# Performance work log

Measured on AMD Instinct MI355X. Metric: run time of the kernel, lower is better.

Reference implementation:

```python
import jax, jax.numpy as jnp
import numpy as np

N_TOK = 384
VOCAB = 50000
N_POS = 52
WDIM = 512
HDIM = 1024
FEAT_DIM = 3 * 16  # np.repeat([len,start,end],16)


def setup_inputs() -> dict:
    key = jax.random.key(0)
    ks = jax.random.split(key, 10)
    s = 0.02  # init scale
    return {
        "sentence": jax.random.randint(ks[0], (N_TOK,), 0, VOCAB),
        "pos_tags": jax.random.randint(ks[1], (N_TOK,), 0, N_POS),
        "We_wrd": jax.random.normal(ks[2], (VOCAB, WDIM), jnp.float32) * s,
        "We_pos": jax.random.normal(ks[3], (N_POS, WDIM), jnp.float32) * s,
        "W_dan1": jax.random.normal(ks[4], (2 * WDIM, HDIM), jnp.float32) * s,
        "b_dan1": jnp.zeros((HDIM,), jnp.float32),
        "W_dan2": jax.random.normal(ks[5], (HDIM, HDIM), jnp.float32) * s,
        "b_dan2": jnp.zeros((HDIM,), jnp.float32),
        "W_s1": jax.random.normal(ks[6], (HDIM + FEAT_DIM, HDIM), jnp.float32) * s,
        "b_s1": jnp.zeros((HDIM,), jnp.float32),
        "W_s2": jax.random.normal(ks[7], (HDIM, 1), jnp.float32) * s,
        "b_s2": jnp.zeros((1,), jnp.float32),
    }


def reference(sentence, pos_tags, We_wrd, We_pos, W_dan1, b_dan1, W_dan2, b_dan2, W_s1, b_s1, W_s2, b_s2):
    n = sentence.shape[0]
    # per-token embedding: concat(pos, word) as in score() with use_pos=True -> [n, 2*wdim]
    emb = jnp.concatenate([We_pos[pos_tags], We_wrd[sentence]], axis=-1)
    # prefix sums so every span mean is O(1): pref[k] = sum of emb[:k]
    pref = jnp.concatenate([jnp.zeros((1, emb.shape[1]), emb.dtype), jnp.cumsum(emb, axis=0)], axis=0)
    # all spans (i, j) with i <= j, as in the double loop over i..n-1, j..n-1
    i_idx, j_idx = np.triu_indices(n)  # static shapes, S = n(n+1)/2
    i_idx = jnp.asarray(i_idx)
    j_idx = jnp.asarray(j_idx)
    end = j_idx + 1
    length = (end - i_idx).astype(emb.dtype)
    # DAN encoder: mean of span embeddings -> 2 relu layers (config['layer']=2)
    mean = (pref[end] - pref[i_idx]) / length[:, None]            # [S, 2*wdim]
    h = jax.nn.relu(mean @ W_dan1 + b_dan1)                        # [S, hdim]
    h = jax.nn.relu(h @ W_dan2 + b_dan2)                           # [S, hdim]
    # phrase feats: np.repeat([len, start, end], 16) -> [S, 48]
    feats = jnp.repeat(jnp.stack([length, i_idx.astype(emb.dtype), end.astype(emb.dtype)], axis=1), 16, axis=1)
    rep = jnp.concatenate([h, feats], axis=1)                      # [S, hdim+48]
    # Wpscore MLP: Linear(ph_dim+48 -> hdim) + relu, Linear(hdim -> 1)
    h2 = jax.nn.relu(rep @ W_s1 + b_s1)
    scores = (h2 @ W_s2 + b_s2)[:, 0]                              # [S]
    return scores
```

## Files before the change

kernel.cpp:

```cpp
#include <hip/hip_runtime.h>

#define NTOK  384
#define SPANS 73920
#define MTILES 584
#define MPAD  (MTILES * 128)
#define HD    1024
#define BK    32
#define KTS   (HD / BK)
#define YSLICE ((size_t)NTOK * HD)

typedef unsigned short u16;
typedef __attribute__((ext_vector_type(8))) short short8;
typedef __attribute__((ext_vector_type(4))) float floatx4;

#define VMCNT_IMM(N) (((N) & 0xF) | (((N) >> 4) << 14) | (0x7 << 4) | (0xF << 8))

__device__ __forceinline__ u16 f2bu(float x) {
  union { float f; unsigned u; } un; un.f = x;
  unsigned r = un.u + 0x7fffu + ((un.u >> 16) & 1u);
  return (u16)(r >> 16);
}

__device__ __forceinline__ void gld_lds16(const void* g, void* l) {
  __builtin_amdgcn_global_load_lds(
      (const __attribute__((address_space(1))) void*)g,
      (__attribute__((address_space(3))) void*)l, 16, 0, 0);
}

__global__ void prep_misc(const int* __restrict__ sent, const int* __restrict__ pos,
                          const float* __restrict__ Wwrd, const float* __restrict__ Wpos,
                          u16* __restrict__ embB,
                          int* __restrict__ spI, int* __restrict__ spE, float* __restrict__ spInv,
                          float* __restrict__ scores, const float* __restrict__ bs2,
                          const float* __restrict__ Wd1, const float* __restrict__ Wd2,
                          const float* __restrict__ Ws1,
                          u16* __restrict__ o1, u16* __restrict__ o2, u16* __restrict__ o3,
                          float* __restrict__ S0, float* __restrict__ S1v, float* __restrict__ S2v) {
  __shared__ u16 tile[32][33];
  int bx = blockIdx.x;
  if (bx < 3072) {
    int w = bx >> 10, rem = bx & 1023;
    int tk = rem >> 5, tn = rem & 31;
    const float* src = (w == 0) ? Wd1 : ((w == 1) ? Wd2 : Ws1);
    u16* dst = (w == 0) ? o1 : ((w == 1) ? o2 : o3);
    int x = threadIdx.x & 31, y = threadIdx.x >> 5;
    int k0 = tk * 32, n0 = tn * 32;
    for (int yy = 0; yy < 32; yy += 8)
      tile[y + yy][x] = f2bu(src[(size_t)(k0 + y + yy) * HD + n0 + x]);
    __syncthreads();
    for (int yy = 0; yy < 32; yy += 8)
      dst[(size_t)(n0 + y + yy) * HD + k0 + x] = tile[x][y + yy];
  } else if (bx < 3072 + NTOK) {
    int t = bx - 3072;
    int c = threadIdx.x;
    int pt = pos[t], st = sent[t];
    #pragma unroll
    for (int u = 0; u < 4; ++u) {
      int col = u * 256 + c;
      float v = (col < 512) ? Wpos[(size_t)pt * 512 + col]
                            : Wwrd[(size_t)st * 512 + (col - 512)];
      embB[(size_t)t * HD + col] = f2bu(v);
    }
  } else if (bx < 3072 + NTOK + 292) {
    int rf = (bx - 3072 - NTOK) * 256 + threadIdx.x;
    if (rf >= MPAD) return;
    int s = rf < SPANS ? rf : SPANS - 1;
    const int n = NTOK;
    double tn2 = 2.0 * n + 1.0;
    int i = (int)((tn2 - sqrt(tn2 * tn2 - 8.0 * (double)s)) * 0.5);
    if (i < 0) i = 0;
    if (i > n - 1) i = n - 1;
    #define OFF(ii) (((ii) * (2 * n - (ii) + 1)) / 2)
    while (i + 1 <= n - 1 && OFF(i + 1) <= s) ++i;
    while (i > 0 && OFF(i) > s) --i;
    int j = i + (s - OFF(i));
    #undef OFF
    spI[rf] = i;
    spE[rf] = j + 1;
    spInv[rf] = 1.0f / (float)(j + 1 - i);
    if (rf < SPANS) scores[rf] = bs2[0];
  } else {
    int c = (bx - 3072 - NTOK - 292) * 256 + threadIdx.x;
    if (c >= HD) return;
    float a = 0.f, b = 0.f, d = 0.f;
    for (int r = 0; r < 16; ++r) {
      a += Ws1[(size_t)(1024 + r) * HD + c];
      b += Ws1[(size_t)(1040 + r) * HD + c];
      d += Ws1[(size_t)(1056 + r) * HD + c];
    }
    S0[c] = a; S1v[c] = b; S2v[c] = d;
  }
}

__global__ void bfrag(const u16* __restrict__ t1, const u16* __restrict__ t2, const u16* __restrict__ t3,
                      u16* __restrict__ f1, u16* __restrict__ f2, u16* __restrict__ f3) {
  int b = blockIdx.x;
  int w = b >> 10, rem = b & 1023;
  int nt = rem >> 5, kt = rem & 31;
  const u16* src = (w == 0) ? t1 : ((w == 1) ? t2 : t3);
  u16* dst = (w == 0) ? f1 : ((w == 1) ? f2 : f3);
  int t = threadIdx.x;
  int ni = t >> 6, lane = t & 63, q = lane >> 4, r = lane & 15;
  #pragma unroll
  for (int wn = 0; wn < 2; ++wn) {
    const u16* s = src + (size_t)(nt * 128 + wn * 64 + ni * 16 + r) * HD + kt * 32 + q * 8;
    u16* d = dst + (size_t)nt * 131072 + kt * 4096 + wn * 2048 + ni * 512 + lane * 8;
    *(short8*)d = *(const short8*)s;
  }
}

__global__ void yscan(const float* __restrict__ Y, float* __restrict__ Qp) {
  __shared__ float buf[NTOK];
  int c = blockIdx.x;
  int t = threadIdx.x;
  size_t idx = (size_t)t * HD + c;
  buf[t] = Y[idx] + Y[idx + YSLICE] + Y[idx + 2 * YSLICE] + Y[idx + 3 * YSLICE];
  __syncthreads();
  #pragma unroll
  for (int off = 1; off < NTOK; off <<= 1) {
    float add = (t >= off) ? buf[t - off] : 0.f;
    __syncthreads();
    buf[t] += add;
    __syncthreads();
  }
  if (t == 0) Qp[c] = 0.f;
  Qp[(size_t)(t + 1) * HD + c] = buf[t];
}

__global__ void expand(const float* __restrict__ Qp, const int* __restrict__ spI,
                       const int* __restrict__ spE, const float* __restrict__ spInv,
                       const float* __restrict__ b1, u16* __restrict__ out) {
  int gid = blockIdx.x * 256 + threadIdx.x;
  int row = gid >> 7;
  int c0 = (gid & 127) << 3;
  int i = spI[row], e = spE[row];
  float inv = spInv[row];
  const float* pe = Qp + (size_t)e * HD + c0;
  const float* pi = Qp + (size_t)i * HD + c0;
  const float* bb = b1 + c0;
  u16 tmp[8];
  #pragma unroll
  for (int u = 0; u < 8; ++u) {
    float v = (pe[u] - pi[u]) * inv + bb[u];
    v = v > 0.f ? v : 0.f;
    tmp[u] = f2bu(v);
  }
  *(uint4*)(out + (size_t)row * HD + c0) = *(const uint4*)tmp;
}

template <int EPI>
__global__ __launch_bounds__(256, 4) void gemm_bt(
    const u16* __restrict__ A, const u16* __restrict__ Bf,
    const float* __restrict__ bias, u16* __restrict__ C, float* __restrict__ Cf,
    const int* __restrict__ spI, const int* __restrict__ spE,
    const float* __restrict__ S0, const float* __restrict__ S1v, const float* __restrict__ S2v,
    const float* __restrict__ Ws2, float* __restrict__ scores) {
  __shared__ u16 As[2][128 * BK];
  int bx = blockIdx.x;
  int mt, nt, ks = 0, KT0 = 0, KT1 = KTS;
  if (EPI == 2) {
    int rem = bx & 31;
    nt = rem & 7; ks = rem >> 3; mt = bx >> 5;
    KT0 = ks * 8; KT1 = KT0 + 8;
  } else {
    int xcd = bx & 7, k = bx >> 3;
    nt = k & 7;
    mt = xcd + 8 * (k >> 3);
  }
  int m0 = mt * 128;
  int n0 = nt * 128;
  int t = threadIdx.x, lane = t & 63, wid = t >> 6;
  int wm = wid >> 1, wn = wid & 1;
  int q = lane >> 4, r = lane & 15;

  floatx4 acc[4][4] = {};

  int dsub = (lane & 7) ^ ((lane >> 3) & 7);
  int row0 = wid * 16 + 2 * (lane >> 3) + (dsub >> 2);
  int voff = row0 * HD + (dsub & 3) * 8;
  const u16* gA0 = A + (size_t)m0 * HD;
  int ldsOff0 = wid * 512;
  int ldsOff1 = 2048 + wid * 512;

  auto stageA = [&](int kt, int b) {
    const u16* pa = gA0 + voff + kt * BK;
    gld_lds16(pa,                   &As[b][ldsOff0]);
    gld_lds16(pa + (size_t)64 * HD, &As[b][ldsOff1]);
  };

  const u16* gBb = Bf + (size_t)nt * 131072 + wn * 2048 + lane * 8;
  auto loadB = [&](int kt, short8 (&bf)[4]) {
    #pragma unroll
    for (int ni = 0; ni < 4; ++ni)
      bf[ni] = *(const short8*)(gBb + (size_t)kt * 4096 + ni * 512);
  };

  int oct = (((r & 1) << 2) + q) ^ ((r >> 1) & 7);
  int aoff[4];
  #pragma unroll
  for (int x = 0; x < 4; ++x)
    aoff[x] = (wm * 32 + x * 8 + (r >> 1)) * 64 + oct * 8;

  short8 af[4], bfA[4], bfB[4];
  auto preloadA = [&](int b) {
    #pragma unroll
    for (int x = 0; x < 4; ++x) af[x] = *(const short8*)(&As[b][aoff[x]]);
  };
  auto burst = [&](short8 (&bf)[4]) {
    #pragma unroll
    for (int ni = 0; ni < 4; ++ni)
      #pragma unroll
      for (int mi = 0; mi < 4; ++mi)
        acc[mi][ni] = __builtin_amdgcn_mfma_f32_16x16x32_bf16(af[mi], bf[ni], acc[mi][ni], 0, 0, 0);
  };

  stageA(KT0, 0);
  stageA(KT0 + 1, 1);
  loadB(KT0, bfA);
  loadB(KT0 + 1, bfB);
  __builtin_amdgcn_s_waitcnt(VMCNT_IMM(0));
  __builtin_amdgcn_s_barrier();
  preloadA(0);

  #pragma unroll 1
  for (int kt = KT0; kt < KT1; kt += 2) {
    burst(bfA);
    __builtin_amdgcn_s_waitcnt(VMCNT_IMM(0));
    __builtin_amdgcn_s_barrier();
    if (kt + 2 < KT1) { stageA(kt + 2, 0); loadB(kt + 2, bfA); }
    preloadA(1);
    burst(bfB);
    __builtin_amdgcn_s_waitcnt(VMCNT_IMM(0));
    __builtin_amdgcn_s_barrier();
    if (kt + 3 < KT1) { stageA(kt + 3, 1); loadB(kt + 3, bfB); }
    if (kt + 2 < KT1) preloadA(0);
  }

  if (EPI == 2) {
    float* Cfk = Cf + (size_t)ks * YSLICE;
    #pragma unroll
    for (int mi = 0; mi < 4; ++mi) {
      int rowb = m0 + wm * 64 + mi * 16 + q * 4;
      #pragma unroll
      for (int ni = 0; ni < 4; ++ni) {
        int col = n0 + wn * 64 + ni * 16 + r;
        #pragma unroll
        for (int e = 0; e < 4; ++e)
          Cfk[(size_t)(rowb + e) * HD + col] = acc[mi][ni][e];
      }
    }
  } else if (EPI == 0) {
    #pragma unroll
    for (int mi = 0; mi < 4; ++mi) {
      int rowb = m0 + wm * 64 + mi * 16 + q * 4;
      #pragma unroll
      for (int ni = 0; ni < 4; ++ni) {
        int col = n0 + wn * 64 + ni * 16 + r;
        float bcol = bias[col];
        #pragma unroll
        for (int e = 0; e < 4; ++e) {
          float v = acc[mi][ni][e] + bcol;
          v = v > 0.f ? v : 0.f;
          C[(size_t)(rowb + e) * HD + col] = f2bu(v);
        }
      }
    }
  } else {
    float bcol[4], s0c[4], s1c[4], s2c[4], wsc[4];
    #pragma unroll
    for (int ni = 0; ni < 4; ++ni) {
      int col = n0 + wn * 64 + ni * 16 + r;
      bcol[ni] = bias[col]; s0c[ni] = S0[col]; s1c[ni] = S1v[col];
      s2c[ni] = S2v[col];  wsc[ni] = Ws2[col];
    }
    #pragma unroll
    for (int mi = 0; mi < 4; ++mi) {
      int rowb = m0 + wm * 64 + mi * 16 + q * 4;
      #pragma unroll
      for (int e = 0; e < 4; ++e) {
        int row = rowb + e;
        float fi = (float)spI[row];
        float fe = (float)spE[row];
        float fl = fe - fi;
        float p = 0.f;
        #pragma unroll
        for (int ni = 0; ni < 4; ++ni) {
          float v = acc[mi][ni][e] + bcol[ni] + fl * s0c[ni] + fi * s1c[ni] + fe * s2c[ni];
          v = v > 0.f ? v : 0.f;
          p += v * wsc[ni];
        }
        p += __shfl_xor(p, 1);
        p += __shfl_xor(p, 2);
        p += __shfl_xor(p, 4);
        p += __shfl_xor(p, 8);
        if (r == 0 && row < SPANS) atomicAdd(&scores[row], p);
      }
    }
  }
}

extern "C" void kernel_launch(void* const* d_in, const int* in_sizes, int n_in,
                              void* d_out, int out_size, void* d_ws, size_t ws_size,
                              hipStream_t stream) {
  const int*   sent = (const int*)d_in[0];
  const int*   pos  = (const int*)d_in[1];
  const float* Wwrd = (const float*)d_in[2];
  const float* Wpos = (const float*)d_in[3];
  const float* Wd1  = (const float*)d_in[4];
  const float* bd1  = (const float*)d_in[5];
  const float* Wd2  = (const float*)d_in[6];
  const float* bd2  = (const float*)d_in[7];
  const float* Ws1  = (const float*)d_in[8];
  const float* bs1  = (const float*)d_in[9];
  const float* Ws2  = (const float*)d_in[10];
  const float* bs2  = (const float*)d_in[11];
  float* scores = (float*)d_out;

  char* w = (char*)d_ws;
  size_t o = 0;
  auto alloc = [&](size_t bytes) {
    char* p = w + o;
    o = (o + bytes + 255) & ~(size_t)255;
    return p;
  };
  int*   spI   = (int*)  alloc((size_t)MPAD * 4);
  int*   spE   = (int*)  alloc((size_t)MPAD * 4);
  float* spInv = (float*)alloc((size_t)MPAD * 4);
  float* S0    = (float*)alloc(4096);
  float* S1v   = (float*)alloc(4096);
  float* S2v   = (float*)alloc(4096);
  u16*   embB  = (u16*)  alloc((size_t)NTOK * HD * 2);
  float* Ybuf  = (float*)alloc(4 * YSLICE * 4);
  float* Qp    = (float*)alloc((size_t)(NTOK + 1) * HD * 4);
  u16* Wd1t = (u16*)alloc((size_t)HD * HD * 2);
  u16* Wd2t = (u16*)alloc((size_t)HD * HD * 2);
  u16* Ws1t = (u16*)alloc((size_t)HD * HD * 2);
  u16* Wd1f = (u16*)alloc((size_t)HD * HD * 2);
  u16* Wd2f = (u16*)alloc((size_t)HD * HD * 2);
  u16* Ws1f = (u16*)alloc((size_t)HD * HD * 2);
  u16* bufA = (u16*)alloc((size_t)MPAD * HD * 2);
  u16* bufB = (u16*)alloc((size_t)MPAD * HD * 2);

  prep_misc<<<3072 + NTOK + 292 + 4, 256, 0, stream>>>(
      sent, pos, Wwrd, Wpos, embB,
      spI, spE, spInv, scores, bs2,
      Wd1, Wd2, Ws1, Wd1t, Wd2t, Ws1t,
      S0, S1v, S2v);
  bfrag<<<3072, 256, 0, stream>>>(Wd1t, Wd2t, Ws1t, Wd1f, Wd2f, Ws1f);

  gemm_bt<2><<<96, 256, 0, stream>>>(embB, Wd1f, nullptr, nullptr, Ybuf,
                                     nullptr, nullptr, nullptr, nullptr, nullptr,
                                     nullptr, nullptr);
  yscan<<<HD, NTOK, 0, stream>>>(Ybuf, Qp);
  expand<<<MPAD / 2, 256, 0, stream>>>(Qp, spI, spE, spInv, bd1, bufA);

  gemm_bt<0><<<MTILES * 8, 256, 0, stream>>>(bufA, Wd2f, bd2, bufB, nullptr,
                                             nullptr, nullptr, nullptr, nullptr, nullptr,
                                             nullptr, nullptr);
  gemm_bt<1><<<MTILES * 8, 256, 0, stream>>>(bufB, Ws1f, bs1, nullptr, nullptr,
                                             spI, spE, S0, S1v, S2v, Ws2, scores);
}
```

Baseline: 575.5 us.

## Store activations in MFMA fragment order and load A directly to registers

The expand kernel and the first big GEMM epilogue now write their bf16 activations in a pre-swizzled fragment layout, laid out like the weight fragments. The two large GEMMs then load A fragments straight from global memory into registers with contiguous 16-byte loads, dropping LDS staging, the waitcnts and the barriers. The first GEMM is split into its own kernel, and launch bounds drop from 4 to 3 blocks per SM. The risk is more global and L2 traffic, because the A tile is no longer shared through LDS across the waves of a block, and lower occupancy.

```diff
diff --git a/kernel.cpp b/kernel.cpp
--- a/kernel.cpp
+++ b/kernel.cpp
@@ -145,30 +145,20 @@
     v = v > 0.f ? v : 0.f;
     tmp[u] = f2bu(v);
   }
-  *(uint4*)(out + (size_t)row * HD + c0) = *(const uint4*)tmp;
-}
-
-template <int EPI>
-__global__ __launch_bounds__(256, 4) void gemm_bt(
-    const u16* __restrict__ A, const u16* __restrict__ Bf,
-    const float* __restrict__ bias, u16* __restrict__ C, float* __restrict__ Cf,
-    const int* __restrict__ spI, const int* __restrict__ spE,
-    const float* __restrict__ S0, const float* __restrict__ S1v, const float* __restrict__ S2v,
-    const float* __restrict__ Ws2, float* __restrict__ scores) {
+  int mt = row >> 7, wm = (row >> 6) & 1, x = (row >> 4) & 3, r = row & 15;
+  int kt = c0 >> 5, q = (c0 >> 3) & 3;
+  size_t addr = (((size_t)(mt * 32 + kt) * 2 + wm) * 4 + x) * 512 + (q * 16 + r) * 8;
+  *(uint4*)(out + addr) = *(const uint4*)tmp;
+}
+
+__global__ __launch_bounds__(256, 3) void gemm_y(
+    const u16* __restrict__ A, const u16* __restrict__ Bf, float* __restrict__ Cf) {
   __shared__ u16 As[2][128 * BK];
   int bx = blockIdx.x;
-  int mt, nt, ks = 0, KT0 = 0, KT1 = KTS;
-  if (EPI == 2) {
-    int rem = bx & 31;
-    nt = rem & 7; ks = rem >> 3; mt = bx >> 5;
-    KT0 = ks * 8; KT1 = KT0 + 8;
-  } else {
-    int xcd = bx & 7, k = bx >> 3;
-    nt = k & 7;
-    mt = xcd + 8 * (k >> 3);
-  }
-  int m0 = mt * 128;
-  int n0 = nt * 128;
+  int rem = bx & 31;
+  int nt = rem & 7, ks = rem >> 3, mt = bx >> 5;
+  int KT0 = ks * 8, KT1 = KT0 + 8;
+  int m0 = mt * 128, n0 = nt * 128;
   int t = threadIdx.x, lane = t & 63, wid = t >> 6;
   int wm = wid >> 1, wn = wid & 1;
   int q = lane >> 4, r = lane & 15;
@@ -236,32 +226,82 @@
     if (kt + 2 < KT1) preloadA(0);
   }
 
-  if (EPI == 2) {
-    float* Cfk = Cf + (size_t)ks * YSLICE;
-    #pragma unroll
-    for (int mi = 0; mi < 4; ++mi) {
-      int rowb = m0 + wm * 64 + mi * 16 + q * 4;
+  float* Cfk = Cf + (size_t)ks * YSLICE;
+  #pragma unroll
+  for (int mi = 0; mi < 4; ++mi) {
+    int rowb = m0 + wm * 64 + mi * 16 + q * 4;
+    #pragma unroll
+    for (int ni = 0; ni < 4; ++ni) {
+      int col = n0 + wn * 64 + ni * 16 + r;
       #pragma unroll
-      for (int ni = 0; ni < 4; ++ni) {
-        int col = n0 + wn * 64 + ni * 16 + r;
-        #pragma unroll
-        for (int e = 0; e < 4; ++e)
-          Cfk[(size_t)(rowb + e) * HD + col] = acc[mi][ni][e];
-      }
-    }
-  } else if (EPI == 0) {
-    #pragma unroll
-    for (int mi = 0; mi < 4; ++mi) {
-      int rowb = m0 + wm * 64 + mi * 16 + q * 4;
+      for (int e = 0; e < 4; ++e)
+        Cfk[(size_t)(rowb + e) * HD + col] = acc[mi][ni][e];
+    }
+  }
+}
+
+template <int EPI>
+__global__ __launch_bounds__(256, 3) void gemm_nf(
+    const u16* __restrict__ Af, const u16* __restrict__ Bf,
+    const float* __restrict__ bias, u16* __restrict__ Cf,
+    const int* __restrict__ spI, const int* __restrict__ spE,
+    const float* __restrict__ S0, const float* __restrict__ S1v, const float* __restrict__ S2v,
+    const float* __restrict__ Ws2, float* __restrict__ scores) {
+  int bx = blockIdx.x;
+  int xcd = bx & 7, k = bx >> 3;
+  int nt = k & 7;
+  int mt = xcd + 8 * (k >> 3);
+  int t = threadIdx.x, lane = t & 63, wid = t >> 6;
+  int wm = wid >> 1, wn = wid & 1;
+  int q = lane >> 4, r = lane & 15;
+
+  floatx4 acc[4][4] = {};
+
+  const u16* gA = Af + (size_t)mt * 131072 + wm * 2048 + lane * 8;
+  const u16* gB = Bf + (size_t)nt * 131072 + wn * 2048 + lane * 8;
+
+  short8 afA[4], afB[4], bfA[4], bfB[4];
+  auto loadA = [&](int kt, short8 (&af)[4]) {
+    #pragma unroll
+    for (int x = 0; x < 4; ++x) af[x] = *(const short8*)(gA + (size_t)kt * 4096 + x * 512);
+  };
+  auto loadB = [&](int kt, short8 (&bf)[4]) {
+    #pragma unroll
+    for (int ni = 0; ni < 4; ++ni) bf[ni] = *(const short8*)(gB + (size_t)kt * 4096 + ni * 512);
+  };
+  auto burst = [&](short8 (&af)[4], short8 (&bf)[4]) {
+    #pragma unroll
+    for (int ni = 0; ni < 4; ++ni)
       #pragma unroll
-      for (int ni = 0; ni < 4; ++ni) {
-        int col = n0 + wn * 64 + ni * 16 + r;
-        float bcol = bias[col];
+      for (int mi = 0; mi < 4; ++mi)
+        acc[mi][ni] = __builtin_amdgcn_mfma_f32_16x16x32_bf16(af[mi], bf[ni], acc[mi][ni], 0, 0, 0);
+  };
+
+  loadA(0, afA); loadB(0, bfA);
+  loadA(1, afB); loadB(1, bfB);
+  #pragma unroll 1
+  for (int kt = 0; kt < KTS; kt += 2) {
+    burst(afA, bfA);
+    if (kt + 2 < KTS) { loadA(kt + 2, afA); loadB(kt + 2, bfA); }
+    burst(afB, bfB);
+    if (kt + 3 < KTS) { loadA(kt + 3, afB); loadB(kt + 3, bfB); }
+  }
+
+  if (EPI == 0) {
+    #pragma unroll
+    for (int ni = 0; ni < 4; ++ni) {
+      int col = nt * 128 + wn * 64 + ni * 16 + r;
+      float bcol = bias[col];
+      int q2 = (ni & 1) * 2 + (r >> 3);
+      #pragma unroll
+      for (int mi = 0; mi < 4; ++mi) {
+        size_t slab = ((size_t)(mt * 32 + nt * 4 + wn * 2 + (ni >> 1)) * 2 + wm) * 4 + mi;
+        u16* base = Cf + slab * 512 + (size_t)(q2 * 16 + q * 4) * 8 + (r & 7);
         #pragma unroll
         for (int e = 0; e < 4; ++e) {
           float v = acc[mi][ni][e] + bcol;
           v = v > 0.f ? v : 0.f;
-          C[(size_t)(rowb + e) * HD + col] = f2bu(v);
+          base[e * 8] = f2bu(v);
         }
       }
     }
@@ -269,10 +309,11 @@
     float bcol[4], s0c[4], s1c[4], s2c[4], wsc[4];
     #pragma unroll
     for (int ni = 0; ni < 4; ++ni) {
-      int col = n0 + wn * 64 + ni * 16 + r;
+      int col = nt * 128 + wn * 64 + ni * 16 + r;
       bcol[ni] = bias[col]; s0c[ni] = S0[col]; s1c[ni] = S1v[col];
       s2c[ni] = S2v[col];  wsc[ni] = Ws2[col];
     }
+    int m0 = mt * 128;
     #pragma unroll
     for (int mi = 0; mi < 4; ++mi) {
       int rowb = m0 + wm * 64 + mi * 16 + q * 4;
@@ -348,15 +389,13 @@
       S0, S1v, S2v);
   bfrag<<<3072, 256, 0, stream>>>(Wd1t, Wd2t, Ws1t, Wd1f, Wd2f, Ws1f);
 
-  gemm_bt<2><<<96, 256, 0, stream>>>(embB, Wd1f, nullptr, nullptr, Ybuf,
-                                     nullptr, nullptr, nullptr, nullptr, nullptr,
-                                     nullptr, nullptr);
+  gemm_y<<<96, 256, 0, stream>>>(embB, Wd1f, Ybuf);
   yscan<<<HD, NTOK, 0, stream>>>(Ybuf, Qp);
   expand<<<MPAD / 2, 256, 0, stream>>>(Qp, spI, spE, spInv, bd1, bufA);
 
-  gemm_bt<0><<<MTILES * 8, 256, 0, stream>>>(bufA, Wd2f, bd2, bufB, nullptr,
+  gemm_nf<0><<<MTILES * 8, 256, 0, stream>>>(bufA, Wd2f, bd2, bufB,
                                              nullptr, nullptr, nullptr, nullptr, nullptr,
                                              nullptr, nullptr);
-  gemm_bt<1><<<MTILES * 8, 256, 0, stream>>>(bufB, Ws1f, bs1, nullptr, nullptr,
+  gemm_nf<1><<<MTILES * 8, 256, 0, stream>>>(bufB, Ws1f, bs1, nullptr,
                                              spI, spE, S0, S1v, S2v, Ws2, scores);
 }
```

New measurement: 672.5 us. 16.9% more time.
